# Optimization experiments

Measured on AMD Instinct MI355X. Metric: run time of the kernel, lower is better.

Reference implementation:

```python
import jax, jax.numpy as jnp
import numpy as np

B, P, D, H, K = 2, 4096, 128, 4, 16
HD = D // H


def _build_mask(key):
    # diagonal (self) + up to K random neighbors per asset, like set_neighborhoods
    nb = jax.random.randint(key, (P, K), 0, P)
    mask = jnp.zeros((P, P), dtype=bool)
    rows = jnp.arange(P)
    mask = mask.at[rows, rows].set(True)
    mask = mask.at[rows[:, None], nb].set(True)
    return mask


def setup_inputs() -> dict:
    key = jax.random.key(0)
    kx, kq, kk, kv, ko, kn = jax.random.split(key, 6)
    s = 1.0 / np.sqrt(D)
    return {
        "x": jax.random.normal(kx, (B, P, D), dtype=jnp.float32),
        "Wq": jax.random.normal(kq, (D, D), dtype=jnp.float32) * s,
        "Wk": jax.random.normal(kk, (D, D), dtype=jnp.float32) * s,
        "Wv": jax.random.normal(kv, (D, D), dtype=jnp.float32) * s,
        "Wo": jax.random.normal(ko, (D, D), dtype=jnp.float32) * s,
        "mask": _build_mask(kn),
    }


def reference(x, Wq, Wk, Wv, Wo, mask):
    b, p, d = x.shape
    # nn.Linear applies x @ W.T
    q = jnp.einsum("bpd,ed->bpe", x, Wq).reshape(b, p, H, HD).transpose(0, 2, 1, 3)
    k = jnp.einsum("bpd,ed->bpe", x, Wk).reshape(b, p, H, HD).transpose(0, 2, 1, 3)
    v = jnp.einsum("bpd,ed->bpe", x, Wv).reshape(b, p, H, HD).transpose(0, 2, 1, 3)
    scale = jnp.float32(HD) ** 0.5
    scores = jnp.einsum("bhpd,bhqd->bhpq", q, k) / scale  # [B,H,P,P]
    scores = jnp.where(mask[None, None, :, :], scores, -jnp.inf)
    w = jax.nn.softmax(scores, axis=-1)
    w = jnp.nan_to_num(w, nan=0.0)  # rows with no neighbors -> zeros
    ctx = jnp.einsum("bhpq,bhqd->bhpd", w, v)
    ctx = ctx.transpose(0, 2, 1, 3).reshape(b, p, d)
    return jnp.einsum("bpd,ed->bpe", ctx, Wo)
```

## Files before the change

kernel.cpp:

```cpp
#include <hip/hip_runtime.h>
#include <hip/hip_bf16.h>

#define PP     4096
#define BB     2
#define DD     128
#define NH     4
#define HDIM   32
#define MROWS  8192
#define MAXN   24

typedef __attribute__((ext_vector_type(8))) short short8;
typedef __attribute__((ext_vector_type(4))) float floatx4;

__device__ __forceinline__ unsigned short f2bf(float f) {
  __hip_bfloat16 h = __float2bfloat16(f);
  return *reinterpret_cast<unsigned short*>(&h);
}

__device__ __forceinline__ int detect_mode(const unsigned char* mask) {
  bool u8ok = true, f32ok = true;
#pragma unroll
  for (int p = 1; p <= 3; ++p) {
    size_t f = (size_t)p * PP + p;
    u8ok = u8ok && (mask[f] == 1);
    unsigned int dw = reinterpret_cast<const unsigned int*>(mask)[f];
    f32ok = f32ok && (dw == 0x3f800000u);
  }
  return u8ok ? 0 : (f32ok ? 2 : 1);
}

__global__ void compact_kernel(const void* __restrict__ mask,
                               const float4* __restrict__ Wq,
                               const float4* __restrict__ Wk,
                               const float4* __restrict__ Wv,
                               const float4* __restrict__ Wo,
                               int* __restrict__ nbr_idx,
                               int* __restrict__ nbr_cnt,
                               unsigned short* __restrict__ Wb) {
  int p = blockIdx.x;
  int lane = threadIdx.x;

  if (p < 256) {
    int u = p * 64 + lane;
    int m = u >> 12, off = u & 4095;
    const float4* Ws = m == 0 ? Wq : (m == 1 ? Wk : (m == 2 ? Wv : Wo));
    float4 v = Ws[off];
    ushort4 o;
    o.x = f2bf(v.x); o.y = f2bf(v.y); o.z = f2bf(v.z); o.w = f2bf(v.w);
    *reinterpret_cast<ushort4*>(Wb + (size_t)m * DD * DD + (size_t)off * 4) = o;
  }

  int md = detect_mode((const unsigned char*)mask);
  unsigned long long bits = 0ULL;

  if (md == 0) {
    const uint4* base =
        reinterpret_cast<const uint4*>((const unsigned char*)mask + (size_t)p * PP) +
        lane * 4;
#pragma unroll
    for (int c = 0; c < 4; ++c) {
      uint4 v = base[c];
      unsigned int w4[4] = {v.x, v.y, v.z, v.w};
#pragma unroll
      for (int wi = 0; wi < 4; ++wi) {
        unsigned int w = w4[wi];
        unsigned int nz = ((((w & 0x7F7F7F7Fu) + 0x7F7F7F7Fu) | w) & 0x80808080u);
        unsigned int x = (nz >> 7) & 0x01010101u;
        unsigned int b4 = (x | (x >> 7) | (x >> 14) | (x >> 21)) & 0xFu;
        bits |= (unsigned long long)b4 << (c * 16 + wi * 4);
      }
    }
  } else if (md == 1) {
    const uint4* base =
        reinterpret_cast<const uint4*>((const int*)mask + (size_t)p * PP) + lane * 16;
#pragma unroll
    for (int c = 0; c < 16; ++c) {
      uint4 v = base[c];
      unsigned long long b = (v.x ? 1u : 0u) | (v.y ? 2u : 0u) |
                             (v.z ? 4u : 0u) | (v.w ? 8u : 0u);
      bits |= b << (c * 4);
    }
  } else {
    const float4* base =
        reinterpret_cast<const float4*>((const float*)mask + (size_t)p * PP) + lane * 16;
#pragma unroll
    for (int c = 0; c < 16; ++c) {
      float4 v = base[c];
      unsigned long long b = (v.x != 0.f ? 1u : 0u) | (v.y != 0.f ? 2u : 0u) |
                             (v.z != 0.f ? 4u : 0u) | (v.w != 0.f ? 8u : 0u);
      bits |= b << (c * 4);
    }
  }

  int cnt = __popcll(bits);
  int pre = cnt;
#pragma unroll
  for (int d = 1; d < 64; d <<= 1) {
    int t = __shfl_up(pre, d);
    if (lane >= d) pre += t;
  }
  int base_pos = pre - cnt;
  unsigned long long m = bits;
  while (m) {
    int b = __ffsll((long long)m) - 1;
    m &= m - 1;
    if (base_pos < MAXN) nbr_idx[p * MAXN + base_pos] = lane * 64 + b;
    ++base_pos;
  }
  int total = __shfl(pre, 63);
  if (lane == 0) nbr_cnt[p] = total < MAXN ? total : MAXN;
}

__global__ void qkv_kernel(const float* __restrict__ x,
                           const unsigned short* __restrict__ Wb,
                           float* __restrict__ Qf, float* __restrict__ Kf,
                           float* __restrict__ Vf) {
  int tid = threadIdx.x;
  int wv = tid >> 6;
  int lane = tid & 63;
  int lrow = lane & 15;
  int kb = lane >> 4;
  int row0 = blockIdx.x * 16;

  floatx4 acc[3][2];
#pragma unroll
  for (int m = 0; m < 3; ++m)
#pragma unroll
    for (int c = 0; c < 2; ++c) acc[m][c] = (floatx4){0.f, 0.f, 0.f, 0.f};

#pragma unroll
  for (int ks = 0; ks < 4; ++ks) {
    int k0 = ks * 32 + kb * 8;
    const float4* xr = reinterpret_cast<const float4*>(x + (size_t)(row0 + lrow) * DD + k0);
    float4 x0 = xr[0], x1 = xr[1];
    short8 a;
    a[0] = (short)f2bf(x0.x); a[1] = (short)f2bf(x0.y);
    a[2] = (short)f2bf(x0.z); a[3] = (short)f2bf(x0.w);
    a[4] = (short)f2bf(x1.x); a[5] = (short)f2bf(x1.y);
    a[6] = (short)f2bf(x1.z); a[7] = (short)f2bf(x1.w);
#pragma unroll
    for (int m = 0; m < 3; ++m) {
      const unsigned short* W = Wb + (size_t)m * DD * DD;
#pragma unroll
      for (int c = 0; c < 2; ++c) {
        int col_tile = wv * 2 + c;
        short8 bf = *reinterpret_cast<const short8*>(
            W + (size_t)(col_tile * 16 + lrow) * DD + k0);
        acc[m][c] = __builtin_amdgcn_mfma_f32_16x16x32_bf16(a, bf, acc[m][c], 0, 0, 0);
      }
    }
  }
#pragma unroll
  for (int m = 0; m < 3; ++m) {
    float* O = m == 0 ? Qf : (m == 1 ? Kf : Vf);
#pragma unroll
    for (int c = 0; c < 2; ++c)
#pragma unroll
      for (int r = 0; r < 4; ++r)
        O[(size_t)(row0 + kb * 4 + r) * DD + (wv * 2 + c) * 16 + lrow] = acc[m][c][r];
  }
}

__global__ void attn_kernel(const float* __restrict__ Qf,
                            const float* __restrict__ Kf,
                            const float* __restrict__ Vf,
                            const int* __restrict__ nbr_idx,
                            const int* __restrict__ nbr_cnt,
                            unsigned short* __restrict__ ctxb) {
  int tid = threadIdx.x;
  int r = tid >> 7;
  int sub = tid & 127;
  int h = sub >> 5, il = sub & 31;
  int row = blockIdx.x * 2 + r;
  int b = row >> 12, p = row & (PP - 1);
  int bBase = b * PP;

  __shared__ int idx_s[2][MAXN];
  __shared__ int cnt_s[2];
  if (tid < 2) cnt_s[tid] = nbr_cnt[(blockIdx.x * 2 + tid) & (PP - 1)];
  if (tid >= 128 && tid < 128 + 2 * MAXN) {
    int u = tid - 128;
    idx_s[u / MAXN][u % MAXN] = nbr_idx[((blockIdx.x * 2 + u / MAXN) & (PP - 1)) * MAXN + u % MAXN];
  }
  __syncthreads();
  int cnt = cnt_s[r];

  float s = -1e30f;
  if (il < cnt) {
    int j = idx_s[r][il];
    const float4* Qr = reinterpret_cast<const float4*>(Qf + (size_t)row * DD + h * HDIM);
    const float4* Kr =
        reinterpret_cast<const float4*>(Kf + (size_t)(bBase + j) * DD + h * HDIM);
    float acc = 0.f;
#pragma unroll
    for (int c = 0; c < 8; ++c) {
      float4 q = Qr[c], k = Kr[c];
      acc = fmaf(q.x, k.x, acc);
      acc = fmaf(q.y, k.y, acc);
      acc = fmaf(q.z, k.z, acc);
      acc = fmaf(q.w, k.w, acc);
    }
    s = acc * 0.17677669529663689f;
  }
  float mx = s;
  mx = fmaxf(mx, __shfl_xor(mx, 16));
  mx = fmaxf(mx, __shfl_xor(mx, 8));
  mx = fmaxf(mx, __shfl_xor(mx, 4));
  mx = fmaxf(mx, __shfl_xor(mx, 2));
  mx = fmaxf(mx, __shfl_xor(mx, 1));
  float w = (il < cnt) ? __expf(s - mx) : 0.f;
  float l = w;
  l += __shfl_xor(l, 16);
  l += __shfl_xor(l, 8);
  l += __shfl_xor(l, 4);
  l += __shfl_xor(l, 2);
  l += __shfl_xor(l, 1);
  __shared__ float ws_s[2][NH][32];
  ws_s[r][h][il] = w / l;
  __syncthreads();

  float acc = 0.f;
  for (int i = 0; i < cnt; ++i) {
    int j = idx_s[r][i];
    acc = fmaf(ws_s[r][h][i], Vf[(size_t)(bBase + j) * DD + h * HDIM + il], acc);
  }
  ctxb[(size_t)row * DD + h * HDIM + il] = f2bf(acc);
}

__global__ void oproj_kernel(const unsigned short* __restrict__ ctxb,
                             const unsigned short* __restrict__ WoB,
                             float* __restrict__ out) {
  int tid = threadIdx.x;
  int wv = tid >> 6;
  int lane = tid & 63;
  int lrow = lane & 15;
  int kb = lane >> 4;
  int row0 = blockIdx.x * 16;

  floatx4 acc[2];
  acc[0] = (floatx4){0.f, 0.f, 0.f, 0.f};
  acc[1] = (floatx4){0.f, 0.f, 0.f, 0.f};
#pragma unroll
  for (int ks = 0; ks < 4; ++ks) {
    int k0 = ks * 32 + kb * 8;
    short8 a = *reinterpret_cast<const short8*>(ctxb + (size_t)(row0 + lrow) * DD + k0);
#pragma unroll
    for (int c = 0; c < 2; ++c) {
      int col_tile = wv * 2 + c;
      short8 bf = *reinterpret_cast<const short8*>(
          WoB + (size_t)(col_tile * 16 + lrow) * DD + k0);
      acc[c] = __builtin_amdgcn_mfma_f32_16x16x32_bf16(a, bf, acc[c], 0, 0, 0);
    }
  }
#pragma unroll
  for (int c = 0; c < 2; ++c)
#pragma unroll
    for (int r = 0; r < 4; ++r)
      out[(size_t)(row0 + kb * 4 + r) * DD + (wv * 2 + c) * 16 + lrow] = acc[c][r];
}

extern "C" void kernel_launch(void* const* d_in, const int* in_sizes, int n_in,
                              void* d_out, int out_size, void* d_ws, size_t ws_size,
                              hipStream_t stream) {
  const float* x    = (const float*)d_in[0];
  const float* Wq   = (const float*)d_in[1];
  const float* Wk   = (const float*)d_in[2];
  const float* Wv   = (const float*)d_in[3];
  const float* Wo   = (const float*)d_in[4];
  const void*  mask = d_in[5];
  float* out = (float*)d_out;

  char* ws = (char*)d_ws;
  int* nbr_cnt = (int*)(ws + 0);
  int* nbr_idx = (int*)(ws + 16384);
  unsigned short* Wb = (unsigned short*)(ws + 409600);
  float* Qf = (float*)(ws + 540672);
  float* Kf = (float*)(ws + 4734976);
  float* Vf = (float*)(ws + 8929280);
  unsigned short* ctxb = (unsigned short*)(ws + 13123584);

  compact_kernel<<<PP, 64, 0, stream>>>(mask, (const float4*)Wq, (const float4*)Wk,
                                        (const float4*)Wv, (const float4*)Wo,
                                        nbr_idx, nbr_cnt, Wb);
  qkv_kernel<<<MROWS / 16, 256, 0, stream>>>(x, Wb, Qf, Kf, Vf);
  attn_kernel<<<MROWS / 2, 256, 0, stream>>>(Qf, Kf, Vf, nbr_idx, nbr_cnt, ctxb);
  oproj_kernel<<<MROWS / 16, 256, 0, stream>>>(ctxb, Wb + (size_t)3 * DD * DD, out);
}
```

Measured before the change: 54.06 us.

## Store K/V in bf16, widen mask compaction blocks, unroll fixed-length attention loops

K and V projections are now written as bf16 instead of fp32, halving the bytes the gather-heavy attention kernel reads per neighbour. The mask compaction kernel moves to 256 threads per row with a cross-wave prefix sum, and drops the float-mask detection path. Unused neighbour slots are padded with the row's own index so attention can run a fully unrolled MAXN loop without branching on the count. The cost is lower precision on K/V, plus extra loads and FMAs with zero weight for the padded slots.

```diff
diff --git a/kernel.cpp b/kernel.cpp
--- a/kernel.cpp
+++ b/kernel.cpp
@@ -16,17 +16,20 @@
   __hip_bfloat16 h = __float2bfloat16(f);
   return *reinterpret_cast<unsigned short*>(&h);
 }
+__device__ __forceinline__ float bf2f(unsigned short u) {
+  union { unsigned int i; float f; } c;
+  c.i = ((unsigned int)u) << 16;
+  return c.f;
+}
 
 __device__ __forceinline__ int detect_mode(const unsigned char* mask) {
-  bool u8ok = true, f32ok = true;
+  bool u8ok = true;
 #pragma unroll
   for (int p = 1; p <= 3; ++p) {
     size_t f = (size_t)p * PP + p;
     u8ok = u8ok && (mask[f] == 1);
-    unsigned int dw = reinterpret_cast<const unsigned int*>(mask)[f];
-    f32ok = f32ok && (dw == 0x3f800000u);
-  }
-  return u8ok ? 0 : (f32ok ? 2 : 1);
+  }
+  return u8ok ? 0 : 1;
 }
 
 __global__ void compact_kernel(const void* __restrict__ mask,
@@ -38,10 +41,11 @@
                                int* __restrict__ nbr_cnt,
                                unsigned short* __restrict__ Wb) {
   int p = blockIdx.x;
-  int lane = threadIdx.x;
-
-  if (p < 256) {
-    int u = p * 64 + lane;
+  int t = threadIdx.x;
+  int lane = t & 63, wv = t >> 6;
+
+  if (p < 64) {
+    int u = p * 256 + t;
     int m = u >> 12, off = u & 4095;
     const float4* Ws = m == 0 ? Wq : (m == 1 ? Wk : (m == 2 ? Wv : Wo));
     float4 v = Ws[off];
@@ -51,70 +55,66 @@
   }
 
   int md = detect_mode((const unsigned char*)mask);
-  unsigned long long bits = 0ULL;
+  unsigned int bits = 0;
 
   if (md == 0) {
+    uint4 v = reinterpret_cast<const uint4*>((const unsigned char*)mask +
+                                             (size_t)p * PP)[t];
+    unsigned int w4[4] = {v.x, v.y, v.z, v.w};
+#pragma unroll
+    for (int wi = 0; wi < 4; ++wi) {
+      unsigned int w = w4[wi];
+      unsigned int nz = ((((w & 0x7F7F7F7Fu) + 0x7F7F7F7Fu) | w) & 0x80808080u);
+      unsigned int x = (nz >> 7) & 0x01010101u;
+      unsigned int b4 = (x | (x >> 7) | (x >> 14) | (x >> 21)) & 0xFu;
+      bits |= b4 << (wi * 4);
+    }
+  } else {
     const uint4* base =
-        reinterpret_cast<const uint4*>((const unsigned char*)mask + (size_t)p * PP) +
-        lane * 4;
+        reinterpret_cast<const uint4*>((const unsigned int*)mask + (size_t)p * PP) +
+        t * 4;
 #pragma unroll
     for (int c = 0; c < 4; ++c) {
       uint4 v = base[c];
-      unsigned int w4[4] = {v.x, v.y, v.z, v.w};
-#pragma unroll
-      for (int wi = 0; wi < 4; ++wi) {
-        unsigned int w = w4[wi];
-        unsigned int nz = ((((w & 0x7F7F7F7Fu) + 0x7F7F7F7Fu) | w) & 0x80808080u);
-        unsigned int x = (nz >> 7) & 0x01010101u;
-        unsigned int b4 = (x | (x >> 7) | (x >> 14) | (x >> 21)) & 0xFu;
-        bits |= (unsigned long long)b4 << (c * 16 + wi * 4);
-      }
-    }
-  } else if (md == 1) {
-    const uint4* base =
-        reinterpret_cast<const uint4*>((const int*)mask + (size_t)p * PP) + lane * 16;
-#pragma unroll
-    for (int c = 0; c < 16; ++c) {
-      uint4 v = base[c];
-      unsigned long long b = (v.x ? 1u : 0u) | (v.y ? 2u : 0u) |
-                             (v.z ? 4u : 0u) | (v.w ? 8u : 0u);
-      bits |= b << (c * 4);
-    }
-  } else {
-    const float4* base =
-        reinterpret_cast<const float4*>((const float*)mask + (size_t)p * PP) + lane * 16;
-#pragma unroll
-    for (int c = 0; c < 16; ++c) {
-      float4 v = base[c];
-      unsigned long long b = (v.x != 0.f ? 1u : 0u) | (v.y != 0.f ? 2u : 0u) |
-                             (v.z != 0.f ? 4u : 0u) | (v.w != 0.f ? 8u : 0u);
-      bits |= b << (c * 4);
-    }
-  }
-
-  int cnt = __popcll(bits);
+      unsigned int b4 = (v.x ? 1u : 0u) | (v.y ? 2u : 0u) |
+                        (v.z ? 4u : 0u) | (v.w ? 8u : 0u);
+      bits |= b4 << (c * 4);
+    }
+  }
+
+  int cnt = __popc(bits);
   int pre = cnt;
 #pragma unroll
   for (int d = 1; d < 64; d <<= 1) {
-    int t = __shfl_up(pre, d);
-    if (lane >= d) pre += t;
-  }
-  int base_pos = pre - cnt;
-  unsigned long long m = bits;
+    int tt = __shfl_up(pre, d);
+    if (lane >= d) pre += tt;
+  }
+  __shared__ int wsum[4];
+  if (lane == 63) wsum[wv] = pre;
+  __syncthreads();
+  int woff = 0;
+#pragma unroll
+  for (int w = 0; w < 4; ++w)
+    if (w < wv) woff += wsum[w];
+  int base_pos = woff + pre - cnt;
+  unsigned int m = bits;
   while (m) {
-    int b = __ffsll((long long)m) - 1;
+    int b = __ffs(m) - 1;
     m &= m - 1;
-    if (base_pos < MAXN) nbr_idx[p * MAXN + base_pos] = lane * 64 + b;
+    if (base_pos < MAXN) nbr_idx[p * MAXN + base_pos] = t * 16 + b;
     ++base_pos;
   }
-  int total = __shfl(pre, 63);
-  if (lane == 0) nbr_cnt[p] = total < MAXN ? total : MAXN;
+  int total = wsum[0] + wsum[1] + wsum[2] + wsum[3];
+  int cl = total < MAXN ? total : MAXN;
+  if (t == 0) nbr_cnt[p] = cl;
+  if (t >= cl && t < MAXN) nbr_idx[p * MAXN + t] = p;
 }
 
 __global__ void qkv_kernel(const float* __restrict__ x,
                            const unsigned short* __restrict__ Wb,
-                           float* __restrict__ Qf, float* __restrict__ Kf,
-                           float* __restrict__ Vf) {
+                           float* __restrict__ Qf,
+                           unsigned short* __restrict__ Kb,
+                           unsigned short* __restrict__ Vb) {
   int tid = threadIdx.x;
   int wv = tid >> 6;
   int lane = tid & 63;
@@ -151,19 +151,19 @@
     }
   }
 #pragma unroll
-  for (int m = 0; m < 3; ++m) {
-    float* O = m == 0 ? Qf : (m == 1 ? Kf : Vf);
-#pragma unroll
-    for (int c = 0; c < 2; ++c)
-#pragma unroll
-      for (int r = 0; r < 4; ++r)
-        O[(size_t)(row0 + kb * 4 + r) * DD + (wv * 2 + c) * 16 + lrow] = acc[m][c][r];
-  }
+  for (int c = 0; c < 2; ++c)
+#pragma unroll
+    for (int r = 0; r < 4; ++r) {
+      size_t off = (size_t)(row0 + kb * 4 + r) * DD + (wv * 2 + c) * 16 + lrow;
+      Qf[off] = acc[0][c][r];
+      Kb[off] = f2bf(acc[1][c][r]);
+      Vb[off] = f2bf(acc[2][c][r]);
+    }
 }
 
 __global__ void attn_kernel(const float* __restrict__ Qf,
-                            const float* __restrict__ Kf,
-                            const float* __restrict__ Vf,
+                            const unsigned short* __restrict__ Kb,
+                            const unsigned short* __restrict__ Vb,
                             const int* __restrict__ nbr_idx,
                             const int* __restrict__ nbr_cnt,
                             unsigned short* __restrict__ ctxb) {
@@ -172,36 +172,41 @@
   int sub = tid & 127;
   int h = sub >> 5, il = sub & 31;
   int row = blockIdx.x * 2 + r;
-  int b = row >> 12, p = row & (PP - 1);
+  int b = row >> 12;
   int bBase = b * PP;
 
   __shared__ int idx_s[2][MAXN];
   __shared__ int cnt_s[2];
+  __shared__ float ws_s[2][NH][32];
   if (tid < 2) cnt_s[tid] = nbr_cnt[(blockIdx.x * 2 + tid) & (PP - 1)];
   if (tid >= 128 && tid < 128 + 2 * MAXN) {
     int u = tid - 128;
-    idx_s[u / MAXN][u % MAXN] = nbr_idx[((blockIdx.x * 2 + u / MAXN) & (PP - 1)) * MAXN + u % MAXN];
+    idx_s[u / MAXN][u % MAXN] =
+        nbr_idx[((blockIdx.x * 2 + u / MAXN) & (PP - 1)) * MAXN + u % MAXN];
   }
   __syncthreads();
   int cnt = cnt_s[r];
 
-  float s = -1e30f;
-  if (il < cnt) {
-    int j = idx_s[r][il];
-    const float4* Qr = reinterpret_cast<const float4*>(Qf + (size_t)row * DD + h * HDIM);
-    const float4* Kr =
-        reinterpret_cast<const float4*>(Kf + (size_t)(bBase + j) * DD + h * HDIM);
-    float acc = 0.f;
-#pragma unroll
-    for (int c = 0; c < 8; ++c) {
-      float4 q = Qr[c], k = Kr[c];
-      acc = fmaf(q.x, k.x, acc);
-      acc = fmaf(q.y, k.y, acc);
-      acc = fmaf(q.z, k.z, acc);
-      acc = fmaf(q.w, k.w, acc);
-    }
-    s = acc * 0.17677669529663689f;
-  }
+  int slot = il < MAXN ? il : MAXN - 1;
+  int j = idx_s[r][slot];
+  const unsigned short* Kr = Kb + (size_t)(bBase + j) * DD + h * HDIM;
+  const float4* Qr = reinterpret_cast<const float4*>(Qf + (size_t)row * DD + h * HDIM);
+  float acc = 0.f;
+#pragma unroll
+  for (int c = 0; c < 4; ++c) {
+    short8 kk = *reinterpret_cast<const short8*>(Kr + c * 8);
+    float4 q0 = Qr[c * 2], q1 = Qr[c * 2 + 1];
+    acc = fmaf(q0.x, bf2f((unsigned short)kk[0]), acc);
+    acc = fmaf(q0.y, bf2f((unsigned short)kk[1]), acc);
+    acc = fmaf(q0.z, bf2f((unsigned short)kk[2]), acc);
+    acc = fmaf(q0.w, bf2f((unsigned short)kk[3]), acc);
+    acc = fmaf(q1.x, bf2f((unsigned short)kk[4]), acc);
+    acc = fmaf(q1.y, bf2f((unsigned short)kk[5]), acc);
+    acc = fmaf(q1.z, bf2f((unsigned short)kk[6]), acc);
+    acc = fmaf(q1.w, bf2f((unsigned short)kk[7]), acc);
+  }
+  float s = (il < cnt) ? acc * 0.17677669529663689f : -1e30f;
+
   float mx = s;
   mx = fmaxf(mx, __shfl_xor(mx, 16));
   mx = fmaxf(mx, __shfl_xor(mx, 8));
@@ -215,16 +220,17 @@
   l += __shfl_xor(l, 4);
   l += __shfl_xor(l, 2);
   l += __shfl_xor(l, 1);
-  __shared__ float ws_s[2][NH][32];
   ws_s[r][h][il] = w / l;
   __syncthreads();
 
-  float acc = 0.f;
-  for (int i = 0; i < cnt; ++i) {
-    int j = idx_s[r][i];
-    acc = fmaf(ws_s[r][h][i], Vf[(size_t)(bBase + j) * DD + h * HDIM + il], acc);
-  }
-  ctxb[(size_t)row * DD + h * HDIM + il] = f2bf(acc);
+  float acc2 = 0.f;
+#pragma unroll
+  for (int i = 0; i < MAXN; ++i) {
+    int jj = idx_s[r][i];
+    float wgt = ws_s[r][h][i];
+    acc2 = fmaf(wgt, bf2f(Vb[(size_t)(bBase + jj) * DD + h * HDIM + il]), acc2);
+  }
+  ctxb[(size_t)row * DD + h * HDIM + il] = f2bf(acc2);
 }
 
 __global__ void oproj_kernel(const unsigned short* __restrict__ ctxb,
@@ -275,14 +281,14 @@
   int* nbr_idx = (int*)(ws + 16384);
   unsigned short* Wb = (unsigned short*)(ws + 409600);
   float* Qf = (float*)(ws + 540672);
-  float* Kf = (float*)(ws + 4734976);
-  float* Vf = (float*)(ws + 8929280);
-  unsigned short* ctxb = (unsigned short*)(ws + 13123584);
-
-  compact_kernel<<<PP, 64, 0, stream>>>(mask, (const float4*)Wq, (const float4*)Wk,
-                                        (const float4*)Wv, (const float4*)Wo,
-                                        nbr_idx, nbr_cnt, Wb);
-  qkv_kernel<<<MROWS / 16, 256, 0, stream>>>(x, Wb, Qf, Kf, Vf);
-  attn_kernel<<<MROWS / 2, 256, 0, stream>>>(Qf, Kf, Vf, nbr_idx, nbr_cnt, ctxb);
+  unsigned short* Kb = (unsigned short*)(ws + 4734976);
+  unsigned short* Vb = (unsigned short*)(ws + 6832128);
+  unsigned short* ctxb = (unsigned short*)(ws + 8929280);
+
+  compact_kernel<<<PP, 256, 0, stream>>>(mask, (const float4*)Wq, (const float4*)Wk,
+                                         (const float4*)Wv, (const float4*)Wo,
+                                         nbr_idx, nbr_cnt, Wb);
+  qkv_kernel<<<MROWS / 16, 256, 0, stream>>>(x, Wb, Qf, Kb, Vb);
+  attn_kernel<<<MROWS / 2, 256, 0, stream>>>(Qf, Kb, Vb, nbr_idx, nbr_cnt, ctxb);
   oproj_kernel<<<MROWS / 16, 256, 0, stream>>>(ctxb, Wb + (size_t)3 * DD * DD, out);
 }
```

New measurement: 46.75 us. 13.5% less time.
